# Optimization experiments

Measured on AMD Instinct MI355X. Metric: run time of the kernel, lower is better.

Reference implementation:

```python
import jax, jax.numpy as jnp
import numpy as np

DIM = 512
HEADS = 8
HEAD_DIM = DIM // HEADS
SCALE = HEAD_DIM ** -0.5
EPS = 1e-5


def setup_inputs() -> dict:
    key = jax.random.key(0)
    ks = jax.random.split(key, 6)
    B, N, C = 4, 2048, DIM
    x = jax.random.normal(ks[0], (B, N, C), dtype=jnp.float32)
    w_qkv = jax.random.normal(ks[1], (C, 3 * C), dtype=jnp.float32) * (C ** -0.5)
    w_proj = jax.random.normal(ks[2], (C, C), dtype=jnp.float32) * (C ** -0.5)
    b_proj = jax.random.normal(ks[3], (C,), dtype=jnp.float32) * 0.02
    gamma = jnp.ones((C,), dtype=jnp.float32)
    beta = jnp.zeros((C,), dtype=jnp.float32)
    return {"x": x, "w_qkv": w_qkv, "w_proj": w_proj, "b_proj": b_proj,
            "gamma": gamma, "beta": beta}


def reference(x, w_qkv, w_proj, b_proj, gamma, beta):
    B, N, C = x.shape
    # LayerNorm over channel dim
    mu = jnp.mean(x, axis=-1, keepdims=True)
    var = jnp.mean(jnp.square(x - mu), axis=-1, keepdims=True)
    xn = (x - mu) * jax.lax.rsqrt(var + EPS) * gamma + beta
    # QKV projection (fp32, no bias)
    qkv = xn @ w_qkv  # [B, N, 3C]
    qkv = qkv.reshape(B, N, 3, HEADS, HEAD_DIM)
    q = jnp.transpose(qkv[:, :, 0], (0, 2, 1, 3))  # [B, H, N, D]
    k = jnp.transpose(qkv[:, :, 1], (0, 2, 1, 3))
    v = jnp.transpose(qkv[:, :, 2], (0, 2, 1, 3))
    attn = jnp.einsum('bhnd,bhmd->bhnm', q, k) * SCALE
    attn = jax.nn.softmax(attn, axis=-1)
    out = jnp.einsum('bhnm,bhmd->bhnd', attn, v)  # [B, H, N, D]
    out = jnp.transpose(out, (0, 2, 1, 3)).reshape(B, N, C)
    out = out @ w_proj + b_proj
    return x + out
```

## Files before the change

kernel.cpp:

```cpp
#include <hip/hip_runtime.h>
#include <hip/hip_bf16.h>
#include <math.h>

typedef _Float16 f16;
typedef _Float16 half8 __attribute__((ext_vector_type(8)));
typedef _Float16 half4 __attribute__((ext_vector_type(4)));
typedef float f32x4 __attribute__((ext_vector_type(4)));

#define DIMC 512
#define HEADS 8
#define HD 64
#define BB 4
#define NN 2048
#define MM (BB*NN)
#define NQKV (3*DIMC)
#define SCALE 0.125f
#define LOG2E 1.44269504f
#define EPSLN 1e-5f
#define NCHUNK 2

__device__ __forceinline__ void g2l16(const void* g, void* l) {
    __builtin_amdgcn_global_load_lds(
        (const __attribute__((address_space(1))) unsigned int*)g,
        (__attribute__((address_space(3))) unsigned int*)l, 16, 0, 0);
}

__device__ __forceinline__ void ln_rows(const float* __restrict__ x,
                                        const float* __restrict__ gamma,
                                        const float* __restrict__ beta,
                                        f16* __restrict__ xn, int blk) {
    int w = threadIdx.x >> 6;
    int lane = threadIdx.x & 63;
    int row = blk * 4 + w;
    const float* xr = x + (size_t)row * DIMC;
    float4 v0 = ((const float4*)xr)[lane * 2];
    float4 v1 = ((const float4*)xr)[lane * 2 + 1];
    float s = v0.x + v0.y + v0.z + v0.w + v1.x + v1.y + v1.z + v1.w;
#pragma unroll
    for (int off = 1; off < 64; off <<= 1) s += __shfl_xor(s, off);
    float mu = s * (1.0f / DIMC);
    float d0 = v0.x - mu, d1 = v0.y - mu, d2 = v0.z - mu, d3 = v0.w - mu;
    float d4 = v1.x - mu, d5 = v1.y - mu, d6 = v1.z - mu, d7 = v1.w - mu;
    float s2 = d0*d0 + d1*d1 + d2*d2 + d3*d3 + d4*d4 + d5*d5 + d6*d6 + d7*d7;
#pragma unroll
    for (int off = 1; off < 64; off <<= 1) s2 += __shfl_xor(s2, off);
    float rstd = rsqrtf(s2 * (1.0f / DIMC) + EPSLN);
    float4 g0 = ((const float4*)gamma)[lane * 2];
    float4 g1 = ((const float4*)gamma)[lane * 2 + 1];
    float4 b0 = ((const float4*)beta)[lane * 2];
    float4 b1 = ((const float4*)beta)[lane * 2 + 1];
    half8 o;
    o[0] = (f16)(d0 * rstd * g0.x + b0.x);
    o[1] = (f16)(d1 * rstd * g0.y + b0.y);
    o[2] = (f16)(d2 * rstd * g0.z + b0.z);
    o[3] = (f16)(d3 * rstd * g0.w + b0.w);
    o[4] = (f16)(d4 * rstd * g1.x + b1.x);
    o[5] = (f16)(d5 * rstd * g1.y + b1.y);
    o[6] = (f16)(d6 * rstd * g1.z + b1.z);
    o[7] = (f16)(d7 * rstd * g1.w + b1.w);
    ((half8*)(xn + (size_t)row * DIMC))[lane] = o;
}

__device__ __forceinline__ void transp_tile(const float* __restrict__ src,
                                            f16* __restrict__ dst,
                                            int R, int C, int k0, int n0) {
    __shared__ f16 t[32][72];
    int tid = threadIdx.x;
    int rr = tid >> 6, col = tid & 63;
#pragma unroll
    for (int p = 0; p < 8; p++) {
        int r = p * 4 + rr;
        t[r][col] = (f16)src[(size_t)(k0 + r) * C + n0 + col];
    }
    __syncthreads();
    int nl = tid >> 2, kc = (tid & 3) * 8;
    half8 v;
#pragma unroll
    for (int j = 0; j < 8; j++) v[j] = t[kc + j][nl];
    *(half8*)&dst[(size_t)(n0 + nl) * R + k0 + kc] = v;
}

__global__ __launch_bounds__(256) void prep_kernel(const float* __restrict__ x,
                                                   const float* __restrict__ gamma,
                                                   const float* __restrict__ beta,
                                                   const float* __restrict__ wqkv,
                                                   const float* __restrict__ wproj,
                                                   f16* __restrict__ xn,
                                                   f16* __restrict__ wqkvt,
                                                   f16* __restrict__ wprojt) {
    int bid = blockIdx.x;
    if (bid < 2048) {
        ln_rows(x, gamma, beta, xn, bid);
    } else if (bid < 2048 + 384) {
        int b2 = bid - 2048;
        int bx = b2 % 24, by = b2 / 24;
        transp_tile(wqkv, wqkvt, DIMC, NQKV, by * 32, bx * 64);
    } else {
        int b2 = bid - 2048 - 384;
        int bx = b2 % 8, by = b2 / 8;
        transp_tile(wproj, wprojt, DIMC, DIMC, by * 32, bx * 64);
    }
}

__device__ __forceinline__ void gemm128_loop(const char* Ag, const char* Bg,
                                             f16* As, f16* Bs, f32x4 (&acc)[4][4]) {
    int tid = threadIdx.x;
    int w = tid >> 6, lane = tid & 63, l15 = lane & 15, quad = lane >> 4;
    int wy = w >> 1, wx = w & 1;
    int off0 = w * 1024 + lane * 16;
    for (int kk = 0; kk < 16; ++kk) {
        __syncthreads();
#pragma unroll
        for (int c = 0; c < 2; ++c) {
            int off = c * 4096 + off0;
            int row = off >> 6, col = off & 63;
            g2l16(Ag + (size_t)row * 1024 + kk * 64 + col, (char*)As + c * 4096 + w * 1024);
            g2l16(Bg + (size_t)row * 1024 + kk * 64 + col, (char*)Bs + c * 4096 + w * 1024);
        }
        __syncthreads();
        half8 af[4], bf[4];
#pragma unroll
        for (int i = 0; i < 4; ++i) {
            af[i] = *(const half8*)((const char*)As + ((wy * 64 + i * 16 + l15) << 6) + quad * 16);
            bf[i] = *(const half8*)((const char*)Bs + ((wx * 64 + i * 16 + l15) << 6) + quad * 16);
        }
#pragma unroll
        for (int i = 0; i < 4; ++i)
#pragma unroll
            for (int j = 0; j < 4; ++j)
                acc[i][j] = __builtin_amdgcn_mfma_f32_16x16x32_f16(af[i], bf[j], acc[i][j], 0, 0, 0);
    }
}

__global__ __launch_bounds__(256) void gemm_qkv(const f16* __restrict__ xn,
                                                const f16* __restrict__ wt,
                                                f16* __restrict__ qb,
                                                f16* __restrict__ kbuf,
                                                f16* __restrict__ vtb) {
    __shared__ __align__(16) f16 As[128 * 32];
    __shared__ __align__(16) f16 Bs[128 * 32];
    int tid = threadIdx.x;
    int w = tid >> 6, lane = tid & 63, l15 = lane & 15, quad = lane >> 4;
    int wy = w >> 1, wx = w & 1;
    int m0 = blockIdx.y * 128, c0 = blockIdx.x * 128;
    f32x4 acc[4][4] = {};
    gemm128_loop((const char*)(xn + (size_t)m0 * DIMC),
                 (const char*)(wt + (size_t)c0 * DIMC), As, Bs, acc);
    int bx = blockIdx.x;
    if (bx < 8) {
        const float QS = SCALE * LOG2E;
        f16* dst = (bx < 4) ? qb : kbuf;
        float mul = (bx < 4) ? QS : 1.0f;
        int cb = (bx < 4) ? c0 : c0 - DIMC;
#pragma unroll
        for (int i = 0; i < 4; ++i)
#pragma unroll
            for (int j = 0; j < 4; ++j)
#pragma unroll
                for (int r = 0; r < 4; ++r) {
                    int m = m0 + wy * 64 + i * 16 + quad * 4 + r;
                    int c = cb + wx * 64 + j * 16 + l15;
                    int b = m >> 11, n = m & 2047;
                    int h = c >> 6, d = c & 63;
                    dst[(((size_t)(b * HEADS + h)) * NN + n) * HD + d] = (f16)(acc[i][j][r] * mul);
                }
    } else {
        __syncthreads();
        f16* T = (f16*)As + w * 512;
        int cb = c0 - 2 * DIMC;
        int dl = lane >> 2, mp = lane & 3;
#pragma unroll
        for (int i = 0; i < 4; ++i)
#pragma unroll
            for (int j = 0; j < 4; ++j) {
                half4 hv;
#pragma unroll
                for (int r = 0; r < 4; ++r) hv[r] = (f16)acc[i][j][r];
                *(half4*)&T[l15 * 20 + quad * 4] = hv;
                half4 rv = *(half4*)&T[dl * 20 + mp * 4];
                int c = cb + wx * 64 + j * 16 + dl;
                int m = m0 + wy * 64 + i * 16 + mp * 4;
                int b = m >> 11, n = m & 2047;
                int h = c >> 6, d = c & 63;
                *(half4*)&vtb[(((size_t)(b * HEADS + h)) * HD + d) * NN + n] = rv;
            }
    }
}

__global__ __launch_bounds__(256, 4) void attn_kernel(const f16* __restrict__ qb,
                                                      const f16* __restrict__ kbuf,
                                                      const f16* __restrict__ vtb,
                                                      f16* __restrict__ po,
                                                      float* __restrict__ pl) {
    __shared__ __align__(16) f16 KV[9216];
    f16* Ks = KV;
    f16* Vs = KV + 4608;
    int id = blockIdx.x;
    int xcd = id & 7, slot = id >> 3;
    int g = xcd * 8 + (slot >> 4);
    int qt4 = slot & 15;
    int bh = g & 31;
    int chunk = g >> 5;
    int n0 = qt4 * 128;
    int tid = threadIdx.x, w = tid >> 6, lane = tid & 63, l15 = lane & 15, quad = lane >> 4;
    const f16* Kbase = kbuf + (size_t)bh * NN * HD;
    const f16* Vbase = vtb + (size_t)bh * HD * NN;
    const f16* Qbase = qb + (size_t)bh * NN * HD;
    half8 qf[2][2];
#pragma unroll
    for (int qt = 0; qt < 2; ++qt) {
        const f16* qr = Qbase + (size_t)(n0 + w * 32 + qt * 16 + l15) * HD + quad * 8;
        qf[qt][0] = *(const half8*)qr;
        qf[qt][1] = *(const half8*)(qr + 32);
    }
    f32x4 ot[2][4] = {};
    f32x4 lacc[2] = {};
    half4 ones;
#pragma unroll
    for (int j = 0; j < 4; ++j) ones[j] = (f16)1.0f;
    int srow = tid >> 2, part = (tid & 3) * 16;
    int kbeg = chunk * (NN / NCHUNK);
    half8 kp0, kp1, vp0, vp1;
    {
        const f16* kg = Kbase + (size_t)(kbeg + srow) * HD + part;
        kp0 = ((const half8*)kg)[0]; kp1 = ((const half8*)kg)[1];
        const f16* vg = Vbase + (size_t)srow * NN + kbeg + part;
        vp0 = ((const half8*)vg)[0]; vp1 = ((const half8*)vg)[1];
    }
    for (int it = 0; it < NN / NCHUNK / 64; ++it) {
        __syncthreads();
        *(half8*)&Ks[srow * 72 + part] = kp0;
        *(half8*)&Ks[srow * 72 + part + 8] = kp1;
        *(half8*)&Vs[srow * 72 + part] = vp0;
        *(half8*)&Vs[srow * 72 + part + 8] = vp1;
        __syncthreads();
        if (it < NN / NCHUNK / 64 - 1) {
            int kt0 = kbeg + (it + 1) * 64;
            const f16* kg = Kbase + (size_t)(kt0 + srow) * HD + part;
            kp0 = ((const half8*)kg)[0]; kp1 = ((const half8*)kg)[1];
            const f16* vg = Vbase + (size_t)srow * NN + kt0 + part;
            vp0 = ((const half8*)vg)[0]; vp1 = ((const half8*)vg)[1];
        }
        f32x4 s0[4], s1[4];
#pragma unroll
        for (int kt = 0; kt < 4; ++kt) {
            half8 a0 = *(const half8*)&Ks[(kt * 16 + l15) * 72 + quad * 8];
            half8 a1 = *(const half8*)&Ks[(kt * 16 + l15) * 72 + 32 + quad * 8];
            f32x4 z0 = {};
            z0 = __builtin_amdgcn_mfma_f32_16x16x32_f16(a0, qf[0][0], z0, 0, 0, 0);
            z0 = __builtin_amdgcn_mfma_f32_16x16x32_f16(a1, qf[0][1], z0, 0, 0, 0);
            s0[kt] = z0;
            f32x4 z1 = {};
            z1 = __builtin_amdgcn_mfma_f32_16x16x32_f16(a0, qf[1][0], z1, 0, 0, 0);
            z1 = __builtin_amdgcn_mfma_f32_16x16x32_f16(a1, qf[1][1], z1, 0, 0, 0);
            s1[kt] = z1;
        }
        half4 pb[2][4];
#pragma unroll
        for (int kt = 0; kt < 4; ++kt) {
            half4 p0, p1;
#pragma unroll
            for (int r = 0; r < 4; ++r) {
                p0[r] = (f16)__builtin_amdgcn_exp2f(s0[kt][r]);
                p1[r] = (f16)__builtin_amdgcn_exp2f(s1[kt][r]);
            }
            pb[0][kt] = p0;
            pb[1][kt] = p1;
        }
#pragma unroll
        for (int kt = 0; kt < 4; ++kt) {
            lacc[0] = __builtin_amdgcn_mfma_f32_16x16x16f16(ones, pb[0][kt], lacc[0], 0, 0, 0);
            lacc[1] = __builtin_amdgcn_mfma_f32_16x16x16f16(ones, pb[1][kt], lacc[1], 0, 0, 0);
#pragma unroll
            for (int dt = 0; dt < 4; ++dt) {
                half4 av = *(const half4*)&Vs[(dt * 16 + l15) * 72 + kt * 16 + quad * 4];
                ot[0][dt] = __builtin_amdgcn_mfma_f32_16x16x16f16(av, pb[0][kt], ot[0][dt], 0, 0, 0);
                ot[1][dt] = __builtin_amdgcn_mfma_f32_16x16x16f16(av, pb[1][kt], ot[1][dt], 0, 0, 0);
            }
        }
    }
    size_t rowbase = ((size_t)chunk * (BB * HEADS) + bh) * NN;
#pragma unroll
    for (int qt = 0; qt < 2; ++qt) {
        if (quad == 0) pl[rowbase + n0 + w * 32 + qt * 16 + l15] = lacc[qt][0];
    }
    __syncthreads();
    f16* T = KV + w * 2304;
#pragma unroll
    for (int qt = 0; qt < 2; ++qt)
#pragma unroll
        for (int dt = 0; dt < 4; ++dt) {
            half4 hv;
#pragma unroll
            for (int r = 0; r < 4; ++r) hv[r] = (f16)ot[qt][dt][r];
            *(half4*)&T[(qt * 16 + l15) * 72 + dt * 16 + quad * 4] = hv;
        }
    __syncthreads();
#pragma unroll
    for (int j = 0; j < 4; ++j) {
        int nl = j * 8 + (lane >> 3);
        int d8 = (lane & 7) * 8;
        half8 v = *(const half8*)&T[nl * 72 + d8];
        *(half8*)&po[(rowbase + n0 + w * 32 + nl) * HD + d8] = v;
    }
}

__global__ __launch_bounds__(256) void attn_combine(const f16* __restrict__ po,
                                                    const float* __restrict__ pl,
                                                    f16* __restrict__ ao) {
    int gid = blockIdx.x * 256 + threadIdx.x;
    int row = gid >> 3, d0 = (gid & 7) * 8;
    int bh = row >> 11, n = row & 2047;
    const int CS = BB * HEADS * NN;
    float l = 0.f;
#pragma unroll
    for (int c = 0; c < NCHUNK; ++c) l += pl[row + c * CS];
    float inv = 1.0f / l;
    float acc[8] = {};
#pragma unroll
    for (int c = 0; c < NCHUNK; ++c) {
        half8 oc = *(const half8*)&po[((size_t)row + c * CS) * HD + d0];
#pragma unroll
        for (int j = 0; j < 8; ++j) acc[j] += (float)oc[j];
    }
    half8 r;
#pragma unroll
    for (int j = 0; j < 8; ++j) r[j] = (f16)(acc[j] * inv);
    int h = bh & 7, b = bh >> 3;
    *(half8*)&ao[((size_t)(b * NN + n)) * DIMC + h * HD + d0] = r;
}

__global__ __launch_bounds__(256) void gemm_proj(const f16* __restrict__ aob,
                                                 const f16* __restrict__ wt,
                                                 const float* __restrict__ x,
                                                 const float* __restrict__ bias,
                                                 float* __restrict__ out) {
    __shared__ __align__(16) f16 As[128 * 32];
    __shared__ __align__(16) f16 Bs[64 * 32];
    int tid = threadIdx.x;
    int w = tid >> 6, lane = tid & 63, l15 = lane & 15, quad = lane >> 4;
    int m0 = blockIdx.y * 128, c0 = blockIdx.x * 64;
    const char* Ag = (const char*)(aob + (size_t)m0 * DIMC);
    const char* Bg = (const char*)(wt + (size_t)c0 * DIMC);
    f32x4 acc[2][4] = {};
    int off0 = w * 1024 + lane * 16;
    for (int kk = 0; kk < 16; ++kk) {
        __syncthreads();
#pragma unroll
        for (int c = 0; c < 2; ++c) {
            int off = c * 4096 + off0;
            int row = off >> 6, col = off & 63;
            g2l16(Ag + (size_t)row * 1024 + kk * 64 + col, (char*)As + c * 4096 + w * 1024);
        }
        {
            int off = tid * 16;
            int row = off >> 6, col = off & 63;
            g2l16(Bg + (size_t)row * 1024 + kk * 64 + col, (char*)Bs + w * 1024);
        }
        __syncthreads();
        half8 af[2], bf[4];
#pragma unroll
        for (int i = 0; i < 2; ++i)
            af[i] = *(const half8*)((const char*)As + ((w * 32 + i * 16 + l15) << 6) + quad * 16);
#pragma unroll
        for (int j = 0; j < 4; ++j)
            bf[j] = *(const half8*)((const char*)Bs + ((j * 16 + l15) << 6) + quad * 16);
#pragma unroll
        for (int i = 0; i < 2; ++i)
#pragma unroll
            for (int j = 0; j < 4; ++j)
                acc[i][j] = __builtin_amdgcn_mfma_f32_16x16x32_f16(af[i], bf[j], acc[i][j], 0, 0, 0);
    }
#pragma unroll
    for (int i = 0; i < 2; ++i)
#pragma unroll
        for (int j = 0; j < 4; ++j)
#pragma unroll
            for (int r = 0; r < 4; ++r) {
                int m = m0 + w * 32 + i * 16 + quad * 4 + r;
                int c = c0 + j * 16 + l15;
                out[(size_t)m * DIMC + c] = x[(size_t)m * DIMC + c] + bias[c] + acc[i][j][r];
            }
}

extern "C" void kernel_launch(void* const* d_in, const int* in_sizes, int n_in,
                              void* d_out, int out_size, void* d_ws, size_t ws_size,
                              hipStream_t stream) {
    (void)in_sizes; (void)n_in; (void)out_size; (void)ws_size;
    const float* x     = (const float*)d_in[0];
    const float* wqkv  = (const float*)d_in[1];
    const float* wproj = (const float*)d_in[2];
    const float* bproj = (const float*)d_in[3];
    const float* gamma = (const float*)d_in[4];
    const float* beta  = (const float*)d_in[5];
    float* out = (float*)d_out;

    char* ws = (char*)d_ws;
    f16* xn     = (f16*)ws;                 ws += (size_t)MM * DIMC * 2;
    f16* wqkvt  = (f16*)ws;                 ws += (size_t)NQKV * DIMC * 2;
    f16* wprojt = (f16*)ws;                 ws += (size_t)DIMC * DIMC * 2;
    f16* qbuf   = (f16*)ws;                 ws += (size_t)MM * DIMC * 2;
    f16* kbuf   = (f16*)ws;                 ws += (size_t)MM * DIMC * 2;
    f16* vtbuf  = (f16*)ws;                 ws += (size_t)MM * DIMC * 2;
    f16* aobuf  = (f16*)ws;                 ws += (size_t)MM * DIMC * 2;
    f16* po     = (f16*)ws;                 ws += (size_t)NCHUNK * BB * HEADS * NN * HD * 2;
    float* pl   = (float*)ws;               ws += (size_t)NCHUNK * BB * HEADS * NN * sizeof(float);

    prep_kernel<<<2048 + 384 + 128, 256, 0, stream>>>(x, gamma, beta, wqkv, wproj,
                                                      xn, wqkvt, wprojt);
    gemm_qkv<<<dim3(NQKV / 128, MM / 128), 256, 0, stream>>>(xn, wqkvt, qbuf, kbuf, vtbuf);
    attn_kernel<<<NN / 128 * BB * HEADS * NCHUNK, 256, 0, stream>>>(qbuf, kbuf, vtbuf, po, pl);
    attn_combine<<<(BB * HEADS * NN * HD / 8) / 256, 256, 0, stream>>>(po, pl, aobuf);
    gemm_proj<<<dim3(DIMC / 64, MM / 128), 256, 0, stream>>>(aobuf, wprojt, x, bproj, out);
}
```

Before: 167.6 us.

## Drop split-KV chunking and normalize attention output in-kernel, removing combine pass

The attention kernel no longer splits the key range into two chunks. Each block now processes the full 2048-key sequence, divides by the row sum itself and writes directly into the [B,N,C] layout. This removes the attn_combine launch and the round trip of partial outputs and sums through global memory. In exchange the attention grid halves from 1024 to 512 blocks, each with twice the serial work, which lowers parallelism and occupancy on the 256-CU device.

```diff
diff --git a/kernel.cpp b/kernel.cpp
--- a/kernel.cpp
+++ b/kernel.cpp
@@ -17,7 +17,6 @@
 #define SCALE 0.125f
 #define LOG2E 1.44269504f
 #define EPSLN 1e-5f
-#define NCHUNK 2
 
 __device__ __forceinline__ void g2l16(const void* g, void* l) {
     __builtin_amdgcn_global_load_lds(
@@ -190,17 +189,14 @@
 __global__ __launch_bounds__(256, 4) void attn_kernel(const f16* __restrict__ qb,
                                                       const f16* __restrict__ kbuf,
                                                       const f16* __restrict__ vtb,
-                                                      f16* __restrict__ po,
-                                                      float* __restrict__ pl) {
+                                                      f16* __restrict__ ao) {
     __shared__ __align__(16) f16 KV[9216];
     f16* Ks = KV;
     f16* Vs = KV + 4608;
     int id = blockIdx.x;
     int xcd = id & 7, slot = id >> 3;
-    int g = xcd * 8 + (slot >> 4);
+    int bh = xcd * 4 + (slot >> 4);
     int qt4 = slot & 15;
-    int bh = g & 31;
-    int chunk = g >> 5;
     int n0 = qt4 * 128;
     int tid = threadIdx.x, w = tid >> 6, lane = tid & 63, l15 = lane & 15, quad = lane >> 4;
     const f16* Kbase = kbuf + (size_t)bh * NN * HD;
@@ -219,23 +215,22 @@
 #pragma unroll
     for (int j = 0; j < 4; ++j) ones[j] = (f16)1.0f;
     int srow = tid >> 2, part = (tid & 3) * 16;
-    int kbeg = chunk * (NN / NCHUNK);
     half8 kp0, kp1, vp0, vp1;
     {
-        const f16* kg = Kbase + (size_t)(kbeg + srow) * HD + part;
+        const f16* kg = Kbase + (size_t)srow * HD + part;
         kp0 = ((const half8*)kg)[0]; kp1 = ((const half8*)kg)[1];
-        const f16* vg = Vbase + (size_t)srow * NN + kbeg + part;
+        const f16* vg = Vbase + (size_t)srow * NN + part;
         vp0 = ((const half8*)vg)[0]; vp1 = ((const half8*)vg)[1];
     }
-    for (int it = 0; it < NN / NCHUNK / 64; ++it) {
+    for (int it = 0; it < NN / 64; ++it) {
         __syncthreads();
         *(half8*)&Ks[srow * 72 + part] = kp0;
         *(half8*)&Ks[srow * 72 + part + 8] = kp1;
         *(half8*)&Vs[srow * 72 + part] = vp0;
         *(half8*)&Vs[srow * 72 + part + 8] = vp1;
         __syncthreads();
-        if (it < NN / NCHUNK / 64 - 1) {
-            int kt0 = kbeg + (it + 1) * 64;
+        if (it < NN / 64 - 1) {
+            int kt0 = (it + 1) * 64;
             const f16* kg = Kbase + (size_t)(kt0 + srow) * HD + part;
             kp0 = ((const half8*)kg)[0]; kp1 = ((const half8*)kg)[1];
             const f16* vg = Vbase + (size_t)srow * NN + kt0 + part;
@@ -279,10 +274,14 @@
             }
         }
     }
-    size_t rowbase = ((size_t)chunk * (BB * HEADS) + bh) * NN;
+    float inv[2];
 #pragma unroll
     for (int qt = 0; qt < 2; ++qt) {
-        if (quad == 0) pl[rowbase + n0 + w * 32 + qt * 16 + l15] = lacc[qt][0];
+        inv[qt] = 1.0f / lacc[qt][0];
+#pragma unroll
+        for (int dt = 0; dt < 4; ++dt)
+#pragma unroll
+            for (int r = 0; r < 4; ++r) ot[qt][dt][r] *= inv[qt];
     }
     __syncthreads();
     f16* T = KV + w * 2304;
@@ -296,38 +295,14 @@
             *(half4*)&T[(qt * 16 + l15) * 72 + dt * 16 + quad * 4] = hv;
         }
     __syncthreads();
+    int h = bh & 7, b = bh >> 3;
 #pragma unroll
     for (int j = 0; j < 4; ++j) {
         int nl = j * 8 + (lane >> 3);
         int d8 = (lane & 7) * 8;
         half8 v = *(const half8*)&T[nl * 72 + d8];
-        *(half8*)&po[(rowbase + n0 + w * 32 + nl) * HD + d8] = v;
-    }
-}
-
-__global__ __launch_bounds__(256) void attn_combine(const f16* __restrict__ po,
-                                                    const float* __restrict__ pl,
-                                                    f16* __restrict__ ao) {
-    int gid = blockIdx.x * 256 + threadIdx.x;
-    int row = gid >> 3, d0 = (gid & 7) * 8;
-    int bh = row >> 11, n = row & 2047;
-    const int CS = BB * HEADS * NN;
-    float l = 0.f;
-#pragma unroll
-    for (int c = 0; c < NCHUNK; ++c) l += pl[row + c * CS];
-    float inv = 1.0f / l;
-    float acc[8] = {};
-#pragma unroll
-    for (int c = 0; c < NCHUNK; ++c) {
-        half8 oc = *(const half8*)&po[((size_t)row + c * CS) * HD + d0];
-#pragma unroll
-        for (int j = 0; j < 8; ++j) acc[j] += (float)oc[j];
-    }
-    half8 r;
-#pragma unroll
-    for (int j = 0; j < 8; ++j) r[j] = (f16)(acc[j] * inv);
-    int h = bh & 7, b = bh >> 3;
-    *(half8*)&ao[((size_t)(b * NN + n)) * DIMC + h * HD + d0] = r;
+        *(half8*)&ao[((size_t)(b * NN + n0 + w * 32 + nl)) * DIMC + h * HD + d8] = v;
+    }
 }
 
 __global__ __launch_bounds__(256) void gemm_proj(const f16* __restrict__ aob,
@@ -403,13 +378,10 @@
     f16* kbuf   = (f16*)ws;                 ws += (size_t)MM * DIMC * 2;
     f16* vtbuf  = (f16*)ws;                 ws += (size_t)MM * DIMC * 2;
     f16* aobuf  = (f16*)ws;                 ws += (size_t)MM * DIMC * 2;
-    f16* po     = (f16*)ws;                 ws += (size_t)NCHUNK * BB * HEADS * NN * HD * 2;
-    float* pl   = (float*)ws;               ws += (size_t)NCHUNK * BB * HEADS * NN * sizeof(float);
 
     prep_kernel<<<2048 + 384 + 128, 256, 0, stream>>>(x, gamma, beta, wqkv, wproj,
                                                       xn, wqkvt, wprojt);
     gemm_qkv<<<dim3(NQKV / 128, MM / 128), 256, 0, stream>>>(xn, wqkvt, qbuf, kbuf, vtbuf);
-    attn_kernel<<<NN / 128 * BB * HEADS * NCHUNK, 256, 0, stream>>>(qbuf, kbuf, vtbuf, po, pl);
-    attn_combine<<<(BB * HEADS * NN * HD / 8) / 256, 256, 0, stream>>>(po, pl, aobuf);
+    attn_kernel<<<512, 256, 0, stream>>>(qbuf, kbuf, vtbuf, aobuf);
     gemm_proj<<<dim3(DIMC / 64, MM / 128), 256, 0, stream>>>(aobuf, wprojt, x, bproj, out);
 }
```

New measurement: 166.9 us. About the same (-0.4%).

## Double-buffer K/V shared tiles in attention to drop one barrier per iteration

Applied to the files above, without the earlier changes.

The attention kernel's K/V shared-memory staging grows to two buffers. Each iteration writes the next tile into the alternate buffer while computing on the current one, so the loop needs one barrier instead of two. Global prefetch now runs two tiles ahead in registers. Shared memory per block doubles to 36 KB, which may limit occupancy under the four-blocks-per-CU launch bound, and the loop count is hardcoded to 16.

```diff
diff --git a/kernel.cpp b/kernel.cpp
--- a/kernel.cpp
+++ b/kernel.cpp
@@ -192,9 +192,7 @@
                                                       const f16* __restrict__ vtb,
                                                       f16* __restrict__ po,
                                                       float* __restrict__ pl) {
-    __shared__ __align__(16) f16 KV[9216];
-    f16* Ks = KV;
-    f16* Vs = KV + 4608;
+    __shared__ __align__(16) f16 KV[18432];
     int id = blockIdx.x;
     int xcd = id & 7, slot = id >> 3;
     int g = xcd * 8 + (slot >> 4);
@@ -227,25 +225,41 @@
         const f16* vg = Vbase + (size_t)srow * NN + kbeg + part;
         vp0 = ((const half8*)vg)[0]; vp1 = ((const half8*)vg)[1];
     }
-    for (int it = 0; it < NN / NCHUNK / 64; ++it) {
-        __syncthreads();
-        *(half8*)&Ks[srow * 72 + part] = kp0;
-        *(half8*)&Ks[srow * 72 + part + 8] = kp1;
-        *(half8*)&Vs[srow * 72 + part] = vp0;
-        *(half8*)&Vs[srow * 72 + part + 8] = vp1;
-        __syncthreads();
-        if (it < NN / NCHUNK / 64 - 1) {
-            int kt0 = kbeg + (it + 1) * 64;
-            const f16* kg = Kbase + (size_t)(kt0 + srow) * HD + part;
-            kp0 = ((const half8*)kg)[0]; kp1 = ((const half8*)kg)[1];
-            const f16* vg = Vbase + (size_t)srow * NN + kt0 + part;
-            vp0 = ((const half8*)vg)[0]; vp1 = ((const half8*)vg)[1];
+    *(half8*)&KV[srow * 72 + part] = kp0;
+    *(half8*)&KV[srow * 72 + part + 8] = kp1;
+    *(half8*)&KV[9216 + srow * 72 + part] = vp0;
+    *(half8*)&KV[9216 + srow * 72 + part + 8] = vp1;
+    {
+        const f16* kg = Kbase + (size_t)(kbeg + 64 + srow) * HD + part;
+        kp0 = ((const half8*)kg)[0]; kp1 = ((const half8*)kg)[1];
+        const f16* vg = Vbase + (size_t)srow * NN + kbeg + 64 + part;
+        vp0 = ((const half8*)vg)[0]; vp1 = ((const half8*)vg)[1];
+    }
+    __syncthreads();
+    for (int it = 0; it < 16; ++it) {
+        int cur = it & 1;
+        const f16* Ksc = KV + cur * 4608;
+        const f16* Vsc = KV + 9216 + cur * 4608;
+        if (it < 15) {
+            f16* Ksn = KV + (cur ^ 1) * 4608;
+            f16* Vsn = KV + 9216 + (cur ^ 1) * 4608;
+            *(half8*)&Ksn[srow * 72 + part] = kp0;
+            *(half8*)&Ksn[srow * 72 + part + 8] = kp1;
+            *(half8*)&Vsn[srow * 72 + part] = vp0;
+            *(half8*)&Vsn[srow * 72 + part + 8] = vp1;
+            if (it < 14) {
+                int kt0 = kbeg + (it + 2) * 64;
+                const f16* kg = Kbase + (size_t)(kt0 + srow) * HD + part;
+                kp0 = ((const half8*)kg)[0]; kp1 = ((const half8*)kg)[1];
+                const f16* vg = Vbase + (size_t)srow * NN + kt0 + part;
+                vp0 = ((const half8*)vg)[0]; vp1 = ((const half8*)vg)[1];
+            }
         }
         f32x4 s0[4], s1[4];
 #pragma unroll
         for (int kt = 0; kt < 4; ++kt) {
-            half8 a0 = *(const half8*)&Ks[(kt * 16 + l15) * 72 + quad * 8];
-            half8 a1 = *(const half8*)&Ks[(kt * 16 + l15) * 72 + 32 + quad * 8];
+            half8 a0 = *(const half8*)&Ksc[(kt * 16 + l15) * 72 + quad * 8];
+            half8 a1 = *(const half8*)&Ksc[(kt * 16 + l15) * 72 + 32 + quad * 8];
             f32x4 z0 = {};
             z0 = __builtin_amdgcn_mfma_f32_16x16x32_f16(a0, qf[0][0], z0, 0, 0, 0);
             z0 = __builtin_amdgcn_mfma_f32_16x16x32_f16(a1, qf[0][1], z0, 0, 0, 0);
@@ -273,18 +287,18 @@
             lacc[1] = __builtin_amdgcn_mfma_f32_16x16x16f16(ones, pb[1][kt], lacc[1], 0, 0, 0);
 #pragma unroll
             for (int dt = 0; dt < 4; ++dt) {
-                half4 av = *(const half4*)&Vs[(dt * 16 + l15) * 72 + kt * 16 + quad * 4];
+                half4 av = *(const half4*)&Vsc[(dt * 16 + l15) * 72 + kt * 16 + quad * 4];
                 ot[0][dt] = __builtin_amdgcn_mfma_f32_16x16x16f16(av, pb[0][kt], ot[0][dt], 0, 0, 0);
                 ot[1][dt] = __builtin_amdgcn_mfma_f32_16x16x16f16(av, pb[1][kt], ot[1][dt], 0, 0, 0);
             }
         }
+        __syncthreads();
     }
     size_t rowbase = ((size_t)chunk * (BB * HEADS) + bh) * NN;
 #pragma unroll
     for (int qt = 0; qt < 2; ++qt) {
         if (quad == 0) pl[rowbase + n0 + w * 32 + qt * 16 + l15] = lacc[qt][0];
     }
-    __syncthreads();
     f16* T = KV + w * 2304;
 #pragma unroll
     for (int qt = 0; qt < 2; ++qt)
```

Result: no change. 168.0 us (+0.3%).
